# Kernel optimization log

Measured on AMD Instinct MI355X. Metric: run time of the kernel, lower is better.

Reference implementation:

```python
import jax, jax.numpy as jnp
import numpy as np

B, N, C_IN, T = 16, 1024, 2, 12
HID, K_CHEB, KT = 64, 3, 3
OUT, PRED = 32, 12
E = 16384
BN_EPS = 1e-5


def _conv(x, w, b):
    # x: (B,C,N,T), w: (O,I,1,kt) -> (B,O,N,T-kt+1)
    y = jax.lax.conv_general_dilated(x, w, (1, 1), 'VALID',
                                     dimension_numbers=('NCHW', 'OIHW', 'NCHW'))
    return y + b[None, :, None, None]


def temporal_conv(X, w1, b1, w2, b2, w3, b3):
    # X: (B,T,N,C) -> (B,T',N,O) with gated GLU-style conv
    x = jnp.transpose(X, (0, 3, 2, 1))  # (B,C,N,T)
    P = _conv(x, w1, b1)
    Q = jax.nn.sigmoid(_conv(x, w2, b2))
    H = jax.nn.relu(P * Q + _conv(x, w3, b3))
    return jnp.transpose(H, (0, 3, 2, 1))


def cheb_conv(x, edge_index, edge_weight, W, b, num_nodes):
    # x: (B,T,N,H); ChebConv with sym normalization, lambda_max=2 => L_hat = -D^-1/2 A D^-1/2
    row, col = edge_index[0], edge_index[1]
    w = jnp.where(row == col, 0.0, edge_weight)  # remove self loops
    deg = jax.ops.segment_sum(w, row, num_segments=num_nodes)
    dinv = jnp.where(deg > 0, jax.lax.rsqrt(jnp.where(deg > 0, deg, 1.0)), 0.0)
    norm = -(dinv[row] * w * dinv[col])  # (E,)

    def prop(z):  # z: (B,T,N,H) -> L_hat @ z along node axis
        return jnp.zeros_like(z).at[:, :, col, :].add(z[:, :, row, :] * norm[:, None])

    Tx0 = x
    out = jnp.einsum('btnh,hf->btnf', Tx0, W[0])
    Tx1 = prop(x)
    out = out + jnp.einsum('btnh,hf->btnf', Tx1, W[1])
    for k in range(2, W.shape[0]):
        Tx2 = 2.0 * prop(Tx1) - Tx0
        out = out + jnp.einsum('btnh,hf->btnf', Tx2, W[k])
        Tx0, Tx1 = Tx1, Tx2
    return out + b


def setup_inputs() -> dict:
    key = jax.random.key(0)
    ks = jax.random.split(key, 20)
    s = 0.1
    inp = {
        'X': jax.random.normal(ks[0], (B, N, C_IN, T), dtype=jnp.float32),
        'edge_index': jax.random.randint(ks[1], (2, E), 0, N),
        'edge_weight': jax.random.uniform(ks[2], (E,), dtype=jnp.float32),
        # temporal conv 1: C_IN -> HID
        'tc1_w1': s * jax.random.normal(ks[3], (HID, C_IN, 1, KT)),
        'tc1_b1': jnp.zeros((HID,)),
        'tc1_w2': s * jax.random.normal(ks[4], (HID, C_IN, 1, KT)),
        'tc1_b2': jnp.zeros((HID,)),
        'tc1_w3': s * jax.random.normal(ks[5], (HID, C_IN, 1, KT)),
        'tc1_b3': jnp.zeros((HID,)),
        # cheb conv
        'cheb_W': s * jax.random.normal(ks[6], (K_CHEB, HID, HID)),
        'cheb_b': jnp.zeros((HID,)),
        # temporal conv 2: HID -> OUT*PRED
        'tc2_w1': s * jax.random.normal(ks[7], (OUT * PRED, HID, 1, KT)),
        'tc2_b1': jnp.zeros((OUT * PRED,)),
        'tc2_w2': s * jax.random.normal(ks[8], (OUT * PRED, HID, 1, KT)),
        'tc2_b2': jnp.zeros((OUT * PRED,)),
        'tc2_w3': s * jax.random.normal(ks[9], (OUT * PRED, HID, 1, KT)),
        'tc2_b3': jnp.zeros((OUT * PRED,)),
        # batch norm over node channel
        'bn_gamma': jnp.ones((N,)),
        'bn_beta': jnp.zeros((N,)),
    }
    return inp


def reference(X, edge_index, edge_weight,
              tc1_w1, tc1_b1, tc1_w2, tc1_b2, tc1_w3, tc1_b3,
              cheb_W, cheb_b,
              tc2_w1, tc2_b1, tc2_w2, tc2_b2, tc2_w3, tc2_b3,
              bn_gamma, bn_beta):
    Xp = jnp.transpose(X, (0, 3, 1, 2))  # (B,T,N,C_in)
    batch, seq_len, num_nodes, _ = Xp.shape
    T0 = temporal_conv(Xp, tc1_w1, tc1_b1, tc1_w2, tc1_b2, tc1_w3, tc1_b3)  # (B,T-2,N,HID)
    Tg = jax.nn.relu(cheb_conv(T0, edge_index, edge_weight, cheb_W, cheb_b, num_nodes))
    T2 = temporal_conv(Tg, tc2_w1, tc2_b1, tc2_w2, tc2_b2, tc2_w3, tc2_b3)  # (B,T-4,N,OUT*PRED)
    T3 = jnp.transpose(T2, (0, 2, 1, 3))  # (B,N,T'',Cout); BN channel = node
    mean = jnp.mean(T3, axis=(0, 2, 3), keepdims=True)
    var = jnp.var(T3, axis=(0, 2, 3), keepdims=True)
    bn = (T3 - mean) * jax.lax.rsqrt(var + BN_EPS)
    bn = bn * bn_gamma[None, :, None, None] + bn_beta[None, :, None, None]
    T4 = jnp.transpose(bn, (3, 0, 1, 2))[..., -1]  # (Cout,B,N)
    return T4.reshape(seq_len, batch, num_nodes, -1)  # (T,B,N,OUT)
```

## Files before the change

kernel.cpp:

```cpp
#include <hip/hip_runtime.h>


typedef __bf16 bf16;
typedef __bf16 bf16x8 __attribute__((ext_vector_type(8)));
typedef float  f32x4  __attribute__((ext_vector_type(4)));

__device__ __forceinline__ f32x4 mfma16(bf16x8 a, bf16x8 b, f32x4 c) {
  return __builtin_amdgcn_mfma_f32_16x16x32_bf16(a, b, c, 0, 0, 0);
}
__device__ __forceinline__ f32x4 splat4(float v) { f32x4 t = {v, v, v, v}; return t; }

__device__ __forceinline__ void lds_load16(const bf16* g, bf16* l) {
  __builtin_amdgcn_global_load_lds((const __attribute__((address_space(1))) void*)g,
                                   (__attribute__((address_space(3))) void*)l, 16, 0, 0);
}

#define NN 1024
#define EE 16384

__global__ __launch_bounds__(256) void deg_kernel(const int* __restrict__ ei,
                                                  const float* __restrict__ ew,
                                                  float* __restrict__ deg) {
  int e = blockIdx.x * 256 + threadIdx.x;
  int r = ei[e], c = ei[EE + e];
  if (r != c) atomicAdd(&deg[r], ew[e]);
}

__global__ __launch_bounds__(256) void scatterL_kernel(const int* __restrict__ ei,
                                                       const float* __restrict__ ew,
                                                       const float* __restrict__ deg,
                                                       float* __restrict__ Lf) {
  int e = blockIdx.x * 256 + threadIdx.x;
  int r = ei[e], c = ei[EE + e];
  float w = (r == c) ? 0.0f : ew[e];
  float dr = deg[r], dc = deg[c];
  float ir = dr > 0.0f ? rsqrtf(dr) : 0.0f;
  float ic = dc > 0.0f ? rsqrtf(dc) : 0.0f;
  float norm = -(ir * w * ic);
  if (norm != 0.0f) atomicAdd(&Lf[(size_t)c * NN + r], norm);
}

__global__ __launch_bounds__(256) void cvtL_kernel(const float* __restrict__ Lf,
                                                   bf16* __restrict__ Lbf) {
  int i = blockIdx.x * 256 + threadIdx.x;
  Lbf[i] = (bf16)Lf[i];
}

__global__ __launch_bounds__(256) void wprep_kernel(const float* __restrict__ W,
                                                    const float* __restrict__ w21,
                                                    const float* __restrict__ w22,
                                                    const float* __restrict__ w23,
                                                    float* __restrict__ Wc,
                                                    bf16* __restrict__ W2c) {
  int i = blockIdx.x * 256 + threadIdx.x;
  if (i < 12288) {
    int row = i >> 6, j = i & 63;
    int src = row >> 6, h = row & 63;
    float v;
    if (src == 0)      v = W[h * 64 + j] - W[2 * 4096 + h * 64 + j];
    else if (src == 1) v = W[4096 + h * 64 + j];
    else               v = 2.0f * W[2 * 4096 + h * 64 + j];
    Wc[i] = v;
  } else {
    int j2 = i - 12288;
    int c = j2 / 192, k = j2 % 192;
    int og = c / 48, r48 = c % 48;
    int conv = r48 >> 4, oo = r48 & 15;
    int o = og * 16 + oo;
    int kk = k >> 6, h = k & 63;
    const float* ws = (conv == 0) ? w21 : (conv == 1) ? w22 : w23;
    W2c[j2] = (bf16)ws[(o * 64 + h) * 3 + kk];
  }
}

__global__ __launch_bounds__(256) void tc1_kernel(const float* __restrict__ X,
                                                  const float* __restrict__ w1, const float* __restrict__ c1,
                                                  const float* __restrict__ w2, const float* __restrict__ c2,
                                                  const float* __restrict__ w3, const float* __restrict__ c3,
                                                  bf16* __restrict__ zf) {
  int row = blockIdx.y;
  int n = blockIdx.x * 256 + threadIdx.x;
  int h = row & 63, bt = row >> 6;
  int t = bt % 10, b = bt / 10;
  float P = c1[h], Q = c2[h], R = c3[h];
  const float* xb = X + (size_t)(b * 1024 + n) * 24;
  #pragma unroll
  for (int c = 0; c < 2; c++)
    #pragma unroll
    for (int k = 0; k < 3; k++) {
      float xv = xb[c * 12 + t + k];
      int wi = (h * 2 + c) * 3 + k;
      P += xv * w1[wi]; Q += xv * w2[wi]; R += xv * w3[wi];
    }
  float Hv = P * (1.0f / (1.0f + __expf(-Q))) + R;
  Hv = Hv > 0.0f ? Hv : 0.0f;
  zf[(size_t)row * NN + n] = (bf16)Hv;
}

__global__ __launch_bounds__(256) void gemm_bt(const bf16* __restrict__ A,
                                               const bf16* __restrict__ Bt,
                                               bf16* __restrict__ C,
                                               int M, int Nc, int K) {
  __shared__ __align__(16) bf16 As[8192];
  __shared__ __align__(16) bf16 Bs[8192];
  const int tid = threadIdx.x, lane = tid & 63, w = tid >> 6;
  const int wm = w >> 1, wn = w & 1;
  const int m0 = blockIdx.y * 128, n0 = blockIdx.x * 128;
  const int colL = lane & 15, kg = lane >> 4;
  const int rxor = colL & 7;

  f32x4 acc[4][4];
  #pragma unroll
  for (int i = 0; i < 4; i++)
    #pragma unroll
    for (int j = 0; j < 4; j++) acc[i][j] = splat4(0.0f);

  for (int kb = 0; kb < K; kb += 64) {
    if (kb) __syncthreads();
    #pragma unroll
    for (int i = 0; i < 4; i++) {
      int e = (w * 4 + i) * 512 + lane * 8;
      int row = e >> 6, s = (e >> 3) & 7;
      int ksw = ((s ^ (row & 7)) << 3);
      lds_load16(&A[(size_t)(m0 + row) * K + kb + ksw], &As[(w * 4 + i) * 512]);
      lds_load16(&Bt[(size_t)(n0 + row) * K + kb + ksw], &Bs[(w * 4 + i) * 512]);
    }
    __syncthreads();
    #pragma unroll
    for (int kk = 0; kk < 2; kk++) {
      bf16x8 af[4], bfr[4];
      #pragma unroll
      for (int mt = 0; mt < 4; mt++)
        af[mt] = *(const bf16x8*)(&As[(wm * 64 + mt * 16 + colL) * 64 +
                                      (((kk * 4 + kg) ^ rxor) << 3)]);
      #pragma unroll
      for (int nt = 0; nt < 4; nt++)
        bfr[nt] = *(const bf16x8*)(&Bs[(wn * 64 + nt * 16 + colL) * 64 +
                                       (((kk * 4 + kg) ^ rxor) << 3)]);
      #pragma unroll
      for (int mt = 0; mt < 4; mt++)
        #pragma unroll
        for (int nt = 0; nt < 4; nt++)
          acc[mt][nt] = mfma16(af[mt], bfr[nt], acc[mt][nt]);
    }
  }
  #pragma unroll
  for (int mt = 0; mt < 4; mt++)
    #pragma unroll
    for (int nt = 0; nt < 4; nt++) {
      int m = m0 + wm * 64 + mt * 16 + kg * 4;
      int n = n0 + wn * 64 + nt * 16 + colL;
      #pragma unroll
      for (int r = 0; r < 4; r++)
        C[(size_t)(m + r) * Nc + n] = (bf16)acc[mt][nt][r];
    }
}

__global__ __launch_bounds__(256) void combine_kernel(const bf16* __restrict__ zf,
                                                      const bf16* __restrict__ P1f,
                                                      const bf16* __restrict__ P2f,
                                                      const float* __restrict__ Wc,
                                                      const float* __restrict__ chebb,
                                                      bf16* __restrict__ Tg) {
  const int slab = blockIdx.y;
  const int b = slab / 10, t = slab % 10;
  const int lane = threadIdx.x & 63;
  const int jg = __builtin_amdgcn_readfirstlane(threadIdx.x >> 6);
  const int n = blockIdx.x * 64 + lane;

  float acc[16];
  #pragma unroll
  for (int j = 0; j < 16; j++) acc[j] = chebb[jg * 16 + j];

  const size_t zoff = (size_t)(slab * 64) * NN + n;
  #pragma unroll 1
  for (int src = 0; src < 3; src++) {
    const bf16* Z = (src == 0) ? zf : (src == 1) ? P1f : P2f;
    const float* wsrc = Wc + (size_t)(src * 64) * 64 + jg * 16;
    #pragma unroll 4
    for (int h = 0; h < 64; h++) {
      float v = (float)Z[zoff + (size_t)h * NN];
      const float* wr = wsrc + h * 64;
      #pragma unroll
      for (int j = 0; j < 16; j++) acc[j] += v * wr[j];
    }
  }

  bf16 tmp[16];
  #pragma unroll
  for (int j = 0; j < 16; j++) {
    float x = acc[j];
    tmp[j] = (bf16)(x > 0.0f ? x : 0.0f);
  }
  size_t base = (size_t)((n * 16 + b) * 10 + t) * 64 + jg * 16;
  *(bf16x8*)(&Tg[base])     = *(const bf16x8*)(&tmp[0]);
  *(bf16x8*)(&Tg[base + 8]) = *(const bf16x8*)(&tmp[8]);
}

__global__ __launch_bounds__(512) void tc2_kernel(const bf16* __restrict__ Tg,
                                                  const bf16* __restrict__ W2c,
                                                  const float* __restrict__ b1,
                                                  const float* __restrict__ b2,
                                                  const float* __restrict__ b3,
                                                  float* __restrict__ nsum,
                                                  float* __restrict__ nsq,
                                                  bf16* __restrict__ slice) {
  __shared__ __align__(16) char smem[122880];
  bf16* Asm = (bf16*)smem;
  const int rb = blockIdx.x;
  const int b = rb >> 5, tpp = (rb >> 2) & 7, n0 = (rb & 3) << 8;
  const int tid = threadIdx.x, lane = tid & 63, w = tid >> 6;
  const int wm = w >> 1, wn = w & 1;
  const int colL = lane & 15, kg = lane >> 4;
  const int rxor = colL & 7;

  #pragma unroll
  for (int i = 0; i < 12; i++) {
    int fb = w * 12288 + i * 1024 + lane * 16;
    int row = fb / 384;
    int s = (fb % 384) >> 4;
    int koff = (s & ~7) * 8 + (((s & 7) ^ (row & 7)) << 3);
    lds_load16(&Tg[(size_t)((n0 + row) * 16 + b) * 640 + tpp * 64 + koff],
               (bf16*)(smem + w * 12288 + i * 1024));
  }
  auto stageW = [&](int colBase, int ks, int buf) {
    {
      int lc = w * 8 + (lane >> 3);
      int cg = colBase + lc;
      int ksrc = ks * 64 + (((lane & 7) ^ (cg & 7)) << 3);
      lds_load16(&W2c[(size_t)cg * 192 + ksrc],
                 (bf16*)(smem + 98304 + buf * 12288 + w * 1024));
    }
    if (w < 4) {
      int s2 = w + 8;
      int lc = s2 * 8 + (lane >> 3);
      int cg = colBase + lc;
      int ksrc = ks * 64 + (((lane & 7) ^ (cg & 7)) << 3);
      lds_load16(&W2c[(size_t)cg * 192 + ksrc],
                 (bf16*)(smem + 98304 + buf * 12288 + s2 * 1024));
    }
  };
  stageW(0, 0, 0);
  __syncthreads();

  float ssum[4][4], ssq[4][4];
  #pragma unroll
  for (int mt = 0; mt < 4; mt++)
    #pragma unroll
    for (int r = 0; r < 4; r++) { ssum[mt][r] = 0.0f; ssq[mt][r] = 0.0f; }

  #pragma unroll 1
  for (int pass = 0; pass < 12; pass++) {
    const int colBase = pass * 96;
    const int pb = pass & 1;

    f32x4 acc[4][3];
    #pragma unroll
    for (int i = 0; i < 4; i++)
      #pragma unroll
      for (int j = 0; j < 3; j++) acc[i][j] = splat4(0.0f);

    #pragma unroll
    for (int ks = 0; ks < 3; ks++) {
      const int bufCur = pb ^ (ks & 1);
      if (pass < 11 || ks < 2) {
        if (ks < 2) stageW(colBase, ks + 1, bufCur ^ 1);
        else        stageW(colBase + 96, 0, bufCur ^ 1);
      }
      const bf16* Wsb = (const bf16*)(smem + 98304 + bufCur * 12288);
      #pragma unroll
      for (int kk = 0; kk < 2; kk++) {
        bf16x8 af[4], bfr[3];
        #pragma unroll
        for (int mt = 0; mt < 4; mt++)
          af[mt] = *(const bf16x8*)(&Asm[(wm * 64 + mt * 16 + colL) * 192 + ks * 64 +
                                         (((kk * 4 + kg) ^ rxor) << 3)]);
        #pragma unroll
        for (int j = 0; j < 3; j++)
          bfr[j] = *(const bf16x8*)(&Wsb[(wn * 48 + j * 16 + colL) * 64 +
                                         (((kk * 4 + kg) ^ rxor) << 3)]);
        #pragma unroll
        for (int mt = 0; mt < 4; mt++)
          #pragma unroll
          for (int j = 0; j < 3; j++)
            acc[mt][j] = mfma16(af[mt], bfr[j], acc[mt][j]);
      }
      __syncthreads();
    }

    const int o = ((pass * 2 + wn) << 4) + colL;
    const float bv1 = b1[o], bv2 = b2[o], bv3 = b3[o];
    #pragma unroll
    for (int mt = 0; mt < 4; mt++)
      #pragma unroll
      for (int r = 0; r < 4; r++) {
        float pv = acc[mt][0][r] + bv1;
        float qv = acc[mt][1][r] + bv2;
        float rv = acc[mt][2][r] + bv3;
        float h = pv * (1.0f / (1.0f + __expf(-qv))) + rv;
        h = h > 0.0f ? h : 0.0f;
        ssum[mt][r] += h;
        ssq[mt][r] += h * h;
        if (tpp == 7) {
          int n = n0 + wm * 64 + mt * 16 + kg * 4 + r;
          slice[(size_t)((b << 10) + n) * 384 + o] = (bf16)h;
        }
      }
  }

  float* sred = (float*)smem;
  sred[tid] = 0.0f;
  __syncthreads();
  #pragma unroll
  for (int mt = 0; mt < 4; mt++)
    #pragma unroll
    for (int r = 0; r < 4; r++) {
      float s = ssum[mt][r], q = ssq[mt][r];
      #pragma unroll
      for (int d = 1; d < 16; d <<= 1) {
        s += __shfl_xor(s, d);
        q += __shfl_xor(q, d);
      }
      if (colL == 0) {
        int rl = wm * 64 + mt * 16 + kg * 4 + r;
        atomicAdd(&sred[rl * 2], s);
        atomicAdd(&sred[rl * 2 + 1], q);
      }
    }
  __syncthreads();
  if (tid < 256) {
    atomicAdd(&nsum[n0 + tid], sred[tid * 2]);
    atomicAdd(&nsq[n0 + tid], sred[tid * 2 + 1]);
  }
}

__global__ __launch_bounds__(256) void bnstat_kernel(const float* __restrict__ nsum,
                                                     const float* __restrict__ nsq,
                                                     const float* __restrict__ gamma,
                                                     const float* __restrict__ beta,
                                                     float* __restrict__ scoff) {
  int n = blockIdx.x * 256 + threadIdx.x;
  const float inv_cnt = 1.0f / 49152.0f;
  float m = nsum[n] * inv_cnt;
  float var = nsq[n] * inv_cnt - m * m;
  float sc = rsqrtf(var + 1e-5f) * gamma[n];
  scoff[n] = sc;
  scoff[1024 + n] = beta[n] - m * sc;
}

__global__ __launch_bounds__(256) void final_kernel(const bf16* __restrict__ slice,
                                                    const float* __restrict__ scoff,
                                                    float* __restrict__ out) {
  int f = blockIdx.x * 256 + threadIdx.x;
  int c = f >> 14, rem = f & 16383;
  int b = rem >> 10, n = rem & 1023;
  out[f] = (float)slice[(size_t)((b << 10) + n) * 384 + c] * scoff[n] + scoff[1024 + n];
}

extern "C" void kernel_launch(void* const* d_in, const int* in_sizes, int n_in,
                              void* d_out, int out_size, void* d_ws, size_t ws_size,
                              hipStream_t stream) {
  const float* X    = (const float*)d_in[0];
  const int*   ei   = (const int*)d_in[1];
  const float* ew   = (const float*)d_in[2];
  const float* t1w1 = (const float*)d_in[3];
  const float* t1b1 = (const float*)d_in[4];
  const float* t1w2 = (const float*)d_in[5];
  const float* t1b2 = (const float*)d_in[6];
  const float* t1w3 = (const float*)d_in[7];
  const float* t1b3 = (const float*)d_in[8];
  const float* chebW = (const float*)d_in[9];
  const float* chebB = (const float*)d_in[10];
  const float* t2w1 = (const float*)d_in[11];
  const float* t2b1 = (const float*)d_in[12];
  const float* t2w2 = (const float*)d_in[13];
  const float* t2b2 = (const float*)d_in[14];
  const float* t2w3 = (const float*)d_in[15];
  const float* t2b3 = (const float*)d_in[16];
  const float* gamma = (const float*)d_in[17];
  const float* beta  = (const float*)d_in[18];
  float* out = (float*)d_out;

  char* ws = (char*)d_ws;
  float* Lf    = (float*)(ws);
  float* deg   = (float*)(ws + 4194304);
  float* nsum  = (float*)(ws + 4198400);
  float* nsq   = (float*)(ws + 4202496);
  bf16*  Lbf   = (bf16*)(ws + 4210688);
  bf16*  zf    = (bf16*)(ws + 6307840);
  bf16*  P1f   = (bf16*)(ws + 27279360);
  bf16*  P2f   = (bf16*)(ws + 48250880);
  bf16*  Tg    = (bf16*)(ws + 69222400);
  float* Wc    = (float*)(ws + 90193920);
  bf16*  W2c   = (bf16*)(ws + 90243072);
  bf16*  slice = (bf16*)(ws + 90685440);
  float* scoff = (float*)(ws + 103268352);

  hipMemsetAsync(ws, 0, 4206592, stream);

  wprep_kernel<<<912, 256, 0, stream>>>(chebW, t2w1, t2w2, t2w3, Wc, W2c);
  tc1_kernel<<<dim3(4, 10240), 256, 0, stream>>>(X, t1w1, t1b1, t1w2, t1b2, t1w3, t1b3, zf);
  deg_kernel<<<64, 256, 0, stream>>>(ei, ew, deg);
  scatterL_kernel<<<64, 256, 0, stream>>>(ei, ew, deg, Lf);
  cvtL_kernel<<<4096, 256, 0, stream>>>(Lf, Lbf);
  gemm_bt<<<dim3(8, 80), 256, 0, stream>>>(zf, Lbf, P1f, 10240, 1024, 1024);
  gemm_bt<<<dim3(8, 80), 256, 0, stream>>>(P1f, Lbf, P2f, 10240, 1024, 1024);
  combine_kernel<<<dim3(16, 160), 256, 0, stream>>>(zf, P1f, P2f, Wc, chebB, Tg);
  tc2_kernel<<<512, 512, 0, stream>>>(Tg, W2c, t2b1, t2b2, t2b3, nsum, nsq, slice);
  bnstat_kernel<<<4, 256, 0, stream>>>(nsum, nsq, gamma, beta, scoff);
  final_kernel<<<24576, 256, 0, stream>>>(slice, scoff, out);
}
```

Measured before the change: 365.6 us.

## Precompute squared Laplacian and run both propagation GEMMs in one dual kernel

Computes L^2 once with a small 1024x1024 GEMM, using a new transposed bf16 copy of L written by a tiled convert kernel. A dual-output GEMM then produces P1 = z·L and P2 = z·L^2 from a single pass over the activation tile, in place of two dependent large GEMMs. This removes the serial dependency between the two propagations and loads the activations once for both products. The cost is extra LDS per block, 512-thread blocks, and a bf16 rounding of L^2 that changes numerics slightly.

```diff
diff --git a/kernel.cpp b/kernel.cpp
--- a/kernel.cpp
+++ b/kernel.cpp
@@ -40,10 +40,30 @@
   if (norm != 0.0f) atomicAdd(&Lf[(size_t)c * NN + r], norm);
 }
 
-__global__ __launch_bounds__(256) void cvtL_kernel(const float* __restrict__ Lf,
-                                                   bf16* __restrict__ Lbf) {
-  int i = blockIdx.x * 256 + threadIdx.x;
-  Lbf[i] = (bf16)Lf[i];
+__global__ __launch_bounds__(256) void cvtLT_kernel(const float* __restrict__ Lf,
+                                                    bf16* __restrict__ Lbf,
+                                                    bf16* __restrict__ LbfT) {
+  __shared__ bf16 T[128 * 136];
+  const int bi = blockIdx.y, bj = blockIdx.x;
+  const int t = threadIdx.x;
+  #pragma unroll
+  for (int k = 0; k < 16; k++) {
+    int f4 = k * 256 + t;
+    int r = f4 >> 5, c4 = f4 & 31;
+    const float4 v = *(const float4*)(&Lf[(size_t)(bi * 128 + r) * NN + bj * 128 + c4 * 4]);
+    bf16 b4[4] = {(bf16)v.x, (bf16)v.y, (bf16)v.z, (bf16)v.w};
+    *(uint2*)(&Lbf[(size_t)(bi * 128 + r) * NN + bj * 128 + c4 * 4]) = *(uint2*)b4;
+    #pragma unroll
+    for (int q = 0; q < 4; q++) T[(c4 * 4 + q) * 136 + r] = b4[q];
+  }
+  __syncthreads();
+  #pragma unroll
+  for (int k = 0; k < 8; k++) {
+    int idx = k * 256 + t;
+    int rr = idx >> 4, cc = idx & 15;
+    *(bf16x8*)(&LbfT[(size_t)(bj * 128 + rr) * NN + bi * 128 + cc * 8]) =
+        *(const bf16x8*)(&T[rr * 136 + cc * 8]);
+  }
 }
 
 __global__ __launch_bounds__(256) void wprep_kernel(const float* __restrict__ W,
@@ -156,6 +176,71 @@
     }
 }
 
+__global__ __launch_bounds__(512) void gemm_dual(const bf16* __restrict__ A,
+                                                 const bf16* __restrict__ B1t,
+                                                 const bf16* __restrict__ B2t,
+                                                 bf16* __restrict__ C1,
+                                                 bf16* __restrict__ C2,
+                                                 int M, int Nc, int K) {
+  __shared__ __align__(16) bf16 As[8192];
+  __shared__ __align__(16) bf16 B1s[8192];
+  __shared__ __align__(16) bf16 B2s[8192];
+  const int tid = threadIdx.x, lane = tid & 63, w = tid >> 6;
+  const int out = w >> 2, wm = (w >> 1) & 1, wn = w & 1;
+  const int m0 = blockIdx.y * 128, n0 = blockIdx.x * 128;
+  const int colL = lane & 15, kg = lane >> 4;
+  const int rxor = colL & 7;
+
+  f32x4 acc[4][4];
+  #pragma unroll
+  for (int i = 0; i < 4; i++)
+    #pragma unroll
+    for (int j = 0; j < 4; j++) acc[i][j] = splat4(0.0f);
+
+  for (int kb = 0; kb < K; kb += 64) {
+    if (kb) __syncthreads();
+    #pragma unroll
+    for (int i = 0; i < 2; i++) {
+      int e = (w * 2 + i) * 512 + lane * 8;
+      int row = e >> 6, s = (e >> 3) & 7;
+      int ksw = ((s ^ (row & 7)) << 3);
+      lds_load16(&A[(size_t)(m0 + row) * K + kb + ksw], &As[(w * 2 + i) * 512]);
+      lds_load16(&B1t[(size_t)(n0 + row) * K + kb + ksw], &B1s[(w * 2 + i) * 512]);
+      lds_load16(&B2t[(size_t)(n0 + row) * K + kb + ksw], &B2s[(w * 2 + i) * 512]);
+    }
+    __syncthreads();
+    const bf16* Bs = out ? B2s : B1s;
+    #pragma unroll
+    for (int kk = 0; kk < 2; kk++) {
+      bf16x8 af[4], bfr[4];
+      #pragma unroll
+      for (int mt = 0; mt < 4; mt++)
+        af[mt] = *(const bf16x8*)(&As[(wm * 64 + mt * 16 + colL) * 64 +
+                                      (((kk * 4 + kg) ^ rxor) << 3)]);
+      #pragma unroll
+      for (int nt = 0; nt < 4; nt++)
+        bfr[nt] = *(const bf16x8*)(&Bs[(wn * 64 + nt * 16 + colL) * 64 +
+                                       (((kk * 4 + kg) ^ rxor) << 3)]);
+      #pragma unroll
+      for (int mt = 0; mt < 4; mt++)
+        #pragma unroll
+        for (int nt = 0; nt < 4; nt++)
+          acc[mt][nt] = mfma16(af[mt], bfr[nt], acc[mt][nt]);
+    }
+  }
+  bf16* C = out ? C2 : C1;
+  #pragma unroll
+  for (int mt = 0; mt < 4; mt++)
+    #pragma unroll
+    for (int nt = 0; nt < 4; nt++) {
+      int m = m0 + wm * 64 + mt * 16 + kg * 4;
+      int n = n0 + wn * 64 + nt * 16 + colL;
+      #pragma unroll
+      for (int r = 0; r < 4; r++)
+        C[(size_t)(m + r) * Nc + n] = (bf16)acc[mt][nt][r];
+    }
+}
+
 __global__ __launch_bounds__(256) void combine_kernel(const bf16* __restrict__ zf,
                                                       const bf16* __restrict__ P1f,
                                                       const bf16* __restrict__ P2f,
@@ -395,6 +480,8 @@
   bf16*  W2c   = (bf16*)(ws + 90243072);
   bf16*  slice = (bf16*)(ws + 90685440);
   float* scoff = (float*)(ws + 103268352);
+  bf16*  LbfT  = (bf16*)(ws + 103276544);
+  bf16*  L2bf  = (bf16*)(ws + 105373696);
 
   hipMemsetAsync(ws, 0, 4206592, stream);
 
@@ -402,9 +489,9 @@
   tc1_kernel<<<dim3(4, 10240), 256, 0, stream>>>(X, t1w1, t1b1, t1w2, t1b2, t1w3, t1b3, zf);
   deg_kernel<<<64, 256, 0, stream>>>(ei, ew, deg);
   scatterL_kernel<<<64, 256, 0, stream>>>(ei, ew, deg, Lf);
-  cvtL_kernel<<<4096, 256, 0, stream>>>(Lf, Lbf);
-  gemm_bt<<<dim3(8, 80), 256, 0, stream>>>(zf, Lbf, P1f, 10240, 1024, 1024);
-  gemm_bt<<<dim3(8, 80), 256, 0, stream>>>(P1f, Lbf, P2f, 10240, 1024, 1024);
+  cvtLT_kernel<<<dim3(8, 8), 256, 0, stream>>>(Lf, Lbf, LbfT);
+  gemm_bt<<<dim3(8, 8), 256, 0, stream>>>(Lbf, LbfT, L2bf, 1024, 1024, 1024);
+  gemm_dual<<<dim3(8, 80), 512, 0, stream>>>(zf, Lbf, L2bf, P1f, P2f, 10240, 1024, 1024);
   combine_kernel<<<dim3(16, 160), 256, 0, stream>>>(zf, P1f, P2f, Wc, chebB, Tg);
   tc2_kernel<<<512, 512, 0, stream>>>(Tg, W2c, t2b1, t2b2, t2b3, nsum, nsq, slice);
   bnstat_kernel<<<4, 256, 0, stream>>>(nsum, nsq, gamma, beta, scoff);
```

After: 392.0 us. +7.2%, slower.
